# Optimization experiments

Measured on AMD Instinct MI355X. Metric: run time of the kernel, lower is better.

## Reference

```python
import jax, jax.numpy as jnp
import numpy as np

N, C, L, E = 10000, 128, 9, 5  # nodes, channels, (lmax+1)^2, num_elements
INV_SQRT_C = 1.0 / np.sqrt(C).astype(np.float32)


def _sparse(key, shape, p=0.15):
    # mimic the sparsity of e3nn CG coupling (U) tensors
    k1, k2 = jax.random.split(key)
    mask = jax.random.bernoulli(k1, p, shape)
    vals = jax.random.normal(k2, shape, dtype=jnp.float32)
    return jnp.where(mask, vals, 0.0)


def setup_inputs() -> dict:
    key = jax.random.key(0)
    ks = jax.random.split(key, 16)
    node_feats = jax.random.normal(ks[0], (N, C, L), dtype=jnp.float32)
    node_attrs = jax.nn.one_hot(jax.random.randint(ks[1], (N,), 0, E), E, dtype=jnp.float32)
    sc = jax.random.normal(ks[2], (N, 512), dtype=jnp.float32)
    # CG coupling tensors U_nu per output irrep (constant buffers in the torch module)
    # l_out = 0 (d=1): path counts k3=10, k2=3, k1=1
    U3_0 = _sparse(ks[3], (1, L, L, L, 10))
    U2_0 = _sparse(ks[4], (1, L, L, 3))
    U1_0 = _sparse(ks[5], (1, L, 1))
    # l_out = 1 (d=3): path counts k3=12, k2=4, k1=1
    U3_1 = _sparse(ks[6], (3, L, L, L, 12))
    U2_1 = _sparse(ks[7], (3, L, L, 4))
    U1_1 = _sparse(ks[8], (3, L, 1))
    # element-dependent contraction weights: randn(E, k, C) / k  (MACE init)
    w3_0 = jax.random.normal(ks[9], (E, 10, C), dtype=jnp.float32) / 10.0
    w2_0 = jax.random.normal(ks[10], (E, 3, C), dtype=jnp.float32) / 3.0
    w1_0 = jax.random.normal(ks[11], (E, 1, C), dtype=jnp.float32) / 1.0
    w3_1 = jax.random.normal(ks[12], (E, 12, C), dtype=jnp.float32) / 12.0
    w2_1 = jax.random.normal(ks[13], (E, 4, C), dtype=jnp.float32) / 4.0
    w1_1 = jax.random.normal(ks[14], (E, 1, C), dtype=jnp.float32) / 1.0
    # o3.Linear internal weights (one [C,C] block per output irrep)
    kl0, kl1 = jax.random.split(ks[15])
    lin_w0 = jax.random.normal(kl0, (C, C), dtype=jnp.float32)
    lin_w1 = jax.random.normal(kl1, (C, C), dtype=jnp.float32)
    return dict(node_feats=node_feats, node_attrs=node_attrs, sc=sc,
                U3_0=U3_0, U2_0=U2_0, U1_0=U1_0, w3_0=w3_0, w2_0=w2_0, w1_0=w1_0,
                U3_1=U3_1, U2_1=U2_1, U1_1=U1_1, w3_1=w3_1, w2_1=w2_1, w1_1=w1_1,
                lin_w0=lin_w0, lin_w1=lin_w1)


def _contraction(x, y, U3, U2, U1, w3, w2, w1):
    # MACE recursive symmetric contraction, correlation=3.
    # x: [N,C,L] node feats, y: [N,E] one-hot, U_nu: [d, L^nu, k_nu], w_nu: [E,k_nu,C]
    out = jnp.einsum('duvwk,ekc,bcw,be->bcduv', U3, w3, x, y)      # [N,C,d,L,L]
    c2 = jnp.einsum('duvk,ekc,be->bcduv', U2, w2, y) + out
    out = jnp.einsum('bcduv,bcv->bcdu', c2, x)                      # [N,C,d,L]
    c1 = jnp.einsum('duk,ekc,be->bcdu', U1, w1, y) + out
    out = jnp.einsum('bcdu,bcu->bcd', c1, x)                        # [N,C,d]
    return out.reshape(out.shape[0], -1)                            # [N,C*d]


def reference(node_feats, node_attrs, sc,
              U3_0, U2_0, U1_0, w3_0, w2_0, w1_0,
              U3_1, U2_1, U1_1, w3_1, w2_1, w1_1,
              lin_w0, lin_w1):
    # SymmetricContraction: one Contraction per target irrep, concat over irreps
    out0 = _contraction(node_feats, node_attrs, U3_0, U2_0, U1_0, w3_0, w2_0, w1_0)  # [N,C]
    out1 = _contraction(node_feats, node_attrs, U3_1, U2_1, U1_1, w3_1, w2_1, w1_1)  # [N,3C]
    # o3.Linear(target_irreps, target_irreps): per-l channel mixing, 1/sqrt(fan_in)
    y0 = (out0 @ lin_w0) * INV_SQRT_C                                # [N,C]
    x1 = out1.reshape(-1, C, 3)
    y1 = jnp.einsum('bcd,ce->bed', x1, lin_w1) * INV_SQRT_C          # [N,C,3]
    out = jnp.concatenate([y0, y1.reshape(-1, 3 * C)], axis=-1)      # [N,512]
    return out + sc  # use_sc residual
```

## Files before the change

### kernel.cpp

```cpp
#include <hip/hip_runtime.h>


#define CCH 128
#define LDIM 9
#define NE 5
#define BLK 256
#define TSTR 220
#define TGSTR 880
#define U3LDS 8748

__global__ __launch_bounds__(BLK) void count_offs_kernel(
    const float* __restrict__ attrs, int N,
    int* __restrict__ elem, int* __restrict__ gcnt,
    int* __restrict__ offs, int* __restrict__ cur) {
  int n = blockIdx.x * BLK + threadIdx.x;
  int e = 0;
  if (n < N) {
    const float* a = attrs + n * NE;
#pragma unroll
    for (int j = 1; j < NE; ++j)
      if (a[j] > 0.5f) e = j;
    elem[n] = e;
  }
  int lane = threadIdx.x & 63;
#pragma unroll
  for (int k = 0; k < NE; ++k) {
    unsigned long long m = __ballot(n < N && e == k);
    if (m) {
      int leader = __ffsll((long long)m) - 1;
      if (lane == leader) atomicAdd(&gcnt[k], __popcll(m));
    }
  }
  __threadfence();
  __syncthreads();
  if (threadIdx.x == 0) {
    int t = atomicAdd(&gcnt[NE], 1);
    if (t == (int)gridDim.x - 1) {
      int acc = 0;
      for (int k = 0; k < NE; ++k) {
        int ck = atomicAdd(&gcnt[k], 0);
        offs[k] = acc; cur[k] = acc; acc += ck;
      }
      offs[NE] = acc;
    }
  }
}

__global__ __launch_bounds__(BLK) void scatter_kernel(
    const int* __restrict__ elem, int N,
    int* __restrict__ cur, int* __restrict__ order) {
  int n = blockIdx.x * BLK + threadIdx.x;
  if (n >= N) return;
  int e = elem[n];
  int lane = threadIdx.x & 63;
#pragma unroll
  for (int k = 0; k < NE; ++k) {
    if (e == k) {
      unsigned long long m = __ballot(1);
      int cnt = __popcll(m);
      int leader = __ffsll((long long)m) - 1;
      int base = 0;
      if (lane == leader) base = atomicAdd(&cur[k], cnt);
      base = __shfl(base, leader);
      int rank = __popcll(m & ((1ull << lane) - 1ull));
      order[base + rank] = n;
    }
  }
}

__global__ __launch_bounds__(BLK) void table_kernel(
    const float* __restrict__ U3_0, const float* __restrict__ U2_0,
    const float* __restrict__ U1_0, const float* __restrict__ U3_1,
    const float* __restrict__ U2_1, const float* __restrict__ U1_1,
    const float* __restrict__ w3_0, const float* __restrict__ w2_0,
    const float* __restrict__ w1_0, const float* __restrict__ w3_1,
    const float* __restrict__ w2_1, const float* __restrict__ w1_1,
    float* __restrict__ table) {
  const int b = blockIdx.x;
  const int dd = blockIdx.y;
  const int e = b / CCH, c = b % CCH;
  float* Tg = table + (size_t)b * TGSTR + dd * TSTR;
  __shared__ float Us[U3LDS];
  __shared__ float U2s[324];
  __shared__ float R3[729];
  __shared__ float R2[81];
  __shared__ float R1l[9];
  __shared__ float w3l[12], w2l[4];
  const int tid = threadIdx.x;
  const int d = dd - 1;
  const int K3 = (dd == 0) ? 10 : 12;
  const int K2 = (dd == 0) ? 3 : 4;

  if (dd == 0) {
    for (int i = tid; i < 7290; i += BLK) Us[i] = U3_0[i];
    for (int i = tid; i < 243; i += BLK)  U2s[i] = U2_0[i];
    if (tid < 10) w3l[tid] = w3_0[(e * 10 + tid) * CCH + c];
    else if (tid < 13) w2l[tid - 10] = w2_0[(e * 3 + (tid - 10)) * CCH + c];
    if (tid < 9) R1l[tid] = U1_0[tid] * w1_0[e * CCH + c];
  } else {
    for (int i = tid; i < 8748; i += BLK) Us[i] = U3_1[d * 8748 + i];
    for (int i = tid; i < 324; i += BLK)  U2s[i] = U2_1[d * 324 + i];
    if (tid < 12) w3l[tid] = w3_1[(e * 12 + tid) * CCH + c];
    else if (tid < 16) w2l[tid - 12] = w2_1[(e * 4 + (tid - 12)) * CCH + c];
    if (tid < 9) R1l[tid] = U1_1[d * 9 + tid] * w1_1[e * CCH + c];
  }
  __syncthreads();
  for (int r = tid; r < 729; r += BLK) {
    float acc = 0.f;
    for (int k = 0; k < K3; ++k) acc += Us[r * K3 + k] * w3l[k];
    R3[r] = acc;
  }
  for (int q = tid; q < 81; q += BLK) {
    float acc = 0.f;
    for (int k = 0; k < K2; ++k) acc += U2s[q * K2 + k] * w2l[k];
    R2[q] = acc;
  }
  __syncthreads();
  for (int i = tid; i < TSTR; i += BLK) {
    float val = 0.f;
    if (i < 219) {
      int rem = i, u = 0;
      while (rem >= (10 - u) * (11 - u) / 2) {
        rem -= (10 - u) * (11 - u) / 2; ++u;
      }
      if (rem == 0) {
        val = R1l[u];
      } else {
        rem -= 1;
        int v = u;
        while (rem >= 10 - v) { rem -= 10 - v; ++v; }
        if (rem == 0) {
          val = (u == v) ? R2[u * 9 + v] : R2[u * 9 + v] + R2[v * 9 + u];
        } else {
          int w = v + (rem - 1);
          if (u == v && v == w)
            val = R3[(u * 9 + u) * 9 + u];
          else if (u == v)
            val = R3[(u * 9 + u) * 9 + w] + R3[(u * 9 + w) * 9 + u] +
                  R3[(w * 9 + u) * 9 + u];
          else if (v == w)
            val = R3[(u * 9 + v) * 9 + v] + R3[(v * 9 + u) * 9 + v] +
                  R3[(v * 9 + v) * 9 + u];
          else
            val = R3[(u * 9 + v) * 9 + w] + R3[(u * 9 + w) * 9 + v] +
                  R3[(v * 9 + u) * 9 + w] + R3[(v * 9 + w) * 9 + u] +
                  R3[(w * 9 + u) * 9 + v] + R3[(w * 9 + v) * 9 + u];
        }
      }
    }
    Tg[i] = val;
  }
}

__global__ __launch_bounds__(BLK, 8) void contract_kernel(
    const float* __restrict__ feats, const float* __restrict__ table,
    const int* __restrict__ order, const int* __restrict__ offs,
    float* __restrict__ tmp, int NPAD) {
  const int c = blockIdx.x;
  int rem = blockIdx.y;
  int e = -1, pbase = 0, segend = 0;
#pragma unroll
  for (int k = 0; k < NE; ++k) {
    int st = offs[k], en = offs[k + 1];
    int nc = (en - st + BLK - 1) >> 8;
    if (e < 0) {
      if (rem < nc) { e = k; pbase = st + rem * BLK; segend = en; }
      else rem -= nc;
    }
  }
  if (e < 0) return;

  const int p = pbase + threadIdx.x;
  const bool valid = (p < segend);
  const int n = order[valid ? p : (segend - 1)];

  float tf[LDIM];
  {
    const float* xp = feats + ((size_t)n * CCH + c) * LDIM;
#pragma unroll
    for (int q = 0; q < LDIM; ++q) tf[q] = xp[q];
  }

  const float* Tc = table + (size_t)(e * CCH + c) * TGSTR;

#pragma unroll 1
  for (int dd = 0; dd < 4; ++dd) {
    const float* B = Tc + dd * TSTR;
    int idx = 0;
    float acc = 0.f;
#pragma unroll
    for (int u = 0; u < 9; ++u) {
      float inner = B[idx++];
#pragma unroll
      for (int v = u; v < 9; ++v) {
        float Hv = B[idx++];
#pragma unroll
        for (int w = v; w < 9; ++w)
          Hv = fmaf(B[idx++], tf[w], Hv);
        inner = fmaf(Hv, tf[v], inner);
      }
      acc = fmaf(inner, tf[u], acc);
    }
    if (valid) tmp[((size_t)dd * CCH + c) * NPAD + p] = acc;
  }
}

#define NB 16
__global__ __launch_bounds__(BLK, 2) void linear_kernel(
    const float* __restrict__ tmp, const float* __restrict__ W0,
    const float* __restrict__ W1, const float* __restrict__ sc,
    const int* __restrict__ order, float* __restrict__ out, int N, int NPAD) {
  const int p0 = blockIdx.x * NB;
  const int t = threadIdx.x;
  const int wave = t >> 6, lane = t & 63;
  __shared__ __align__(16) float SU[16384];

#pragma unroll
  for (int k = 0; k < 8; ++k) {
    int f = t + k * BLK;
    int dd = f >> 9, r = f & 511;
    int ci = r >> 2, q = r & 3;
    float4 v = *(const float4*)(tmp + (size_t)(dd * CCH + ci) * NPAD + p0 + q * 4);
    *(float4*)(SU + dd * 2048 + ci * 16 + q * 4) = v;
  }
  {
    const int fo0 = wave * 512 + lane * 4;
    const int fo1 = fo0 + 256;
    __builtin_amdgcn_global_load_lds(W0 + fo0, &SU[8192 + fo0], 16, 0, 0);
    __builtin_amdgcn_global_load_lds(W0 + fo1, &SU[8192 + fo1], 16, 0, 0);
    __builtin_amdgcn_global_load_lds(W1 + fo0, &SU[8192 + 2048 + fo0], 16, 0, 0);
    __builtin_amdgcn_global_load_lds(W1 + fo1, &SU[8192 + 2048 + fo1], 16, 0, 0);
  }
  __syncthreads();

  const int j2 = t & 7;
  const int o = t >> 3;
  float acc[2][4][4];
#pragma unroll
  for (int jj = 0; jj < 2; ++jj)
#pragma unroll
    for (int dd = 0; dd < 4; ++dd)
#pragma unroll
      for (int k = 0; k < 4; ++k) acc[jj][dd][k] = 0.f;

#pragma unroll 1
  for (int kk = 0; kk < 8; ++kk) {
    if (kk < 7) {
      const int wb = 8192 + ((kk + 1) & 1) * 4096;
      const float* s0 = W0 + (kk + 1) * 2048;
      const float* s1 = W1 + (kk + 1) * 2048;
      const int fo0 = wave * 512 + lane * 4;
      const int fo1 = fo0 + 256;
      __builtin_amdgcn_global_load_lds(s0 + fo0, &SU[wb + fo0], 16, 0, 0);
      __builtin_amdgcn_global_load_lds(s0 + fo1, &SU[wb + fo1], 16, 0, 0);
      __builtin_amdgcn_global_load_lds(s1 + fo0, &SU[wb + 2048 + fo0], 16, 0, 0);
      __builtin_amdgcn_global_load_lds(s1 + fo1, &SU[wb + 2048 + fo1], 16, 0, 0);
    }
    const int wb = 8192 + (kk & 1) * 4096;
#pragma unroll
    for (int cl = 0; cl < 16; ++cl) {
      const int ci = kk * 16 + cl;
      const float4 wa = *(const float4*)(SU + wb + cl * 128 + o * 4);
      const float4 wc = *(const float4*)(SU + wb + 2048 + cl * 128 + o * 4);
      float av[4][2];
#pragma unroll
      for (int dd = 0; dd < 4; ++dd) {
        av[dd][0] = SU[dd * 2048 + ci * 16 + j2];
        av[dd][1] = SU[dd * 2048 + ci * 16 + j2 + 8];
      }
#pragma unroll
      for (int jj = 0; jj < 2; ++jj) {
        acc[jj][0][0] = fmaf(av[0][jj], wa.x, acc[jj][0][0]);
        acc[jj][0][1] = fmaf(av[0][jj], wa.y, acc[jj][0][1]);
        acc[jj][0][2] = fmaf(av[0][jj], wa.z, acc[jj][0][2]);
        acc[jj][0][3] = fmaf(av[0][jj], wa.w, acc[jj][0][3]);
#pragma unroll
        for (int d = 1; d < 4; ++d) {
          acc[jj][d][0] = fmaf(av[d][jj], wc.x, acc[jj][d][0]);
          acc[jj][d][1] = fmaf(av[d][jj], wc.y, acc[jj][d][1]);
          acc[jj][d][2] = fmaf(av[d][jj], wc.z, acc[jj][d][2]);
          acc[jj][d][3] = fmaf(av[d][jj], wc.w, acc[jj][d][3]);
        }
      }
    }
    __syncthreads();
  }

  const float s = 0.08838834764831843f;
#pragma unroll
  for (int jj = 0; jj < 2; ++jj) {
    float* Sj = SU + (j2 + jj * 8) * 516;
#pragma unroll
    for (int k = 0; k < 4; ++k) {
      int co = o * 4 + k;
      Sj[co]               = acc[jj][0][k] * s;
      Sj[CCH + co * 3 + 0] = acc[jj][1][k] * s;
      Sj[CCH + co * 3 + 1] = acc[jj][2][k] * s;
      Sj[CCH + co * 3 + 2] = acc[jj][3][k] * s;
    }
  }
  __syncthreads();

  const int f = t & 127;
  const int jj4 = t >> 7;
#pragma unroll 1
  for (int jr = jj4; jr < NB; jr += 2) {
    int p = p0 + jr;
    if (p < N) {
      int n = order[p];
      float4 sv = ((const float4*)(sc + (size_t)n * 512))[f];
      float4 ov = ((const float4*)(SU + jr * 516))[f];
      ov.x += sv.x; ov.y += sv.y; ov.z += sv.z; ov.w += sv.w;
      ((float4*)(out + (size_t)n * 512))[f] = ov;
    }
  }
}

extern "C" void kernel_launch(void* const* d_in, const int* in_sizes, int n_in,
                              void* d_out, int out_size, void* d_ws, size_t ws_size,
                              hipStream_t stream) {
  const float* feats = (const float*)d_in[0];
  const float* attrs = (const float*)d_in[1];
  const float* sc    = (const float*)d_in[2];
  const float* U3_0  = (const float*)d_in[3];
  const float* U2_0  = (const float*)d_in[4];
  const float* U1_0  = (const float*)d_in[5];
  const float* w3_0  = (const float*)d_in[6];
  const float* w2_0  = (const float*)d_in[7];
  const float* w1_0  = (const float*)d_in[8];
  const float* U3_1  = (const float*)d_in[9];
  const float* U2_1  = (const float*)d_in[10];
  const float* U1_1  = (const float*)d_in[11];
  const float* w3_1  = (const float*)d_in[12];
  const float* w2_1  = (const float*)d_in[13];
  const float* w1_1  = (const float*)d_in[14];
  const float* W0    = (const float*)d_in[15];
  const float* W1    = (const float*)d_in[16];

  const int N = in_sizes[0] / (CCH * LDIM);
  const int NPAD = ((N + 15) & ~15) + 16;

  float* table = (float*)d_ws;
  float* tmp   = table + (size_t)NE * CCH * TGSTR;
  int*   order = (int*)(tmp + (size_t)4 * CCH * NPAD);
  int*   elem  = order + N;
  int*   offs  = elem + N;
  int*   cur   = offs + 8;
  int*   gcnt  = cur + 8;
  float* out   = (float*)d_out;

  hipMemsetAsync(gcnt, 0, 8 * sizeof(int), stream);

  const int nblk = (N + BLK - 1) / BLK;
  count_offs_kernel<<<dim3(nblk), dim3(BLK), 0, stream>>>(
      attrs, N, elem, gcnt, offs, cur);
  scatter_kernel<<<dim3(nblk), dim3(BLK), 0, stream>>>(elem, N, cur, order);

  table_kernel<<<dim3(NE * CCH, 4), dim3(BLK), 0, stream>>>(
      U3_0, U2_0, U1_0, U3_1, U2_1, U1_1,
      w3_0, w2_0, w1_0, w3_1, w2_1, w1_1, table);

  const int chunksMax = (N + BLK - 1) / BLK + NE;
  contract_kernel<<<dim3(CCH, chunksMax), dim3(BLK), 0, stream>>>(
      feats, table, order, offs, tmp, NPAD);

  linear_kernel<<<dim3((N + NB - 1) / NB), dim3(BLK), 0, stream>>>(
      tmp, W0, W1, sc, order, out, N, NPAD);
}
```

Baseline: 259.5 us.

## Store contraction output node-major and hold linear weights in registers

The contraction kernel now stages its four per-channel results in LDS and writes them as one float4 per node into a node-major [N,512] buffer, replacing the old channel-major padded layout. The linear kernel is rewritten around that layout. Each of 256 blocks of 512 threads owns a contiguous chunk of nodes. Each thread keeps a 128-entry weight column in registers and computes one output per node, reading the intermediate with wave-uniform loads, then adds the skip connection through an LDS row buffer. The aim is to drop the LDS-tiled GEMM staging, but the contraction stores become widely strided across threads. The 128-float register array, under a 512-thread, 2-blocks-per-CU launch bound, risks register spills, and the per-node serial loop gives little parallelism.

```diff
diff --git a/kernel.cpp b/kernel.cpp
--- a/kernel.cpp
+++ b/kernel.cpp
@@ -155,7 +155,7 @@
 __global__ __launch_bounds__(BLK, 8) void contract_kernel(
     const float* __restrict__ feats, const float* __restrict__ table,
     const int* __restrict__ order, const int* __restrict__ offs,
-    float* __restrict__ tmp, int NPAD) {
+    float* __restrict__ tmpT) {
   const int c = blockIdx.x;
   int rem = blockIdx.y;
   int e = -1, pbase = 0, segend = 0;
@@ -174,6 +174,8 @@
   const bool valid = (p < segend);
   const int n = order[valid ? p : (segend - 1)];
 
+  __shared__ float LT[4][BLK];
+
   float tf[LDIM];
   {
     const float* xp = feats + ((size_t)n * CCH + c) * LDIM;
@@ -201,118 +203,84 @@
       }
       acc = fmaf(inner, tf[u], acc);
     }
-    if (valid) tmp[((size_t)dd * CCH + c) * NPAD + p] = acc;
-  }
-}
-
-#define NB 16
-__global__ __launch_bounds__(BLK, 2) void linear_kernel(
-    const float* __restrict__ tmp, const float* __restrict__ W0,
+    LT[dd][threadIdx.x] = acc;
+  }
+  if (valid) {
+    float4 v;
+    v.x = LT[0][threadIdx.x];
+    v.y = LT[1][threadIdx.x];
+    v.z = LT[2][threadIdx.x];
+    v.w = LT[3][threadIdx.x];
+    *(float4*)(tmpT + (size_t)p * 512 + c * 4) = v;
+  }
+}
+
+__global__ __launch_bounds__(512, 2) void linear_kernel(
+    const float* __restrict__ tmpT, const float* __restrict__ W0,
     const float* __restrict__ W1, const float* __restrict__ sc,
-    const int* __restrict__ order, float* __restrict__ out, int N, int NPAD) {
-  const int p0 = blockIdx.x * NB;
+    const int* __restrict__ order, float* __restrict__ out, int N) {
   const int t = threadIdx.x;
-  const int wave = t >> 6, lane = t & 63;
-  __shared__ __align__(16) float SU[16384];
-
-#pragma unroll
-  for (int k = 0; k < 8; ++k) {
-    int f = t + k * BLK;
-    int dd = f >> 9, r = f & 511;
-    int ci = r >> 2, q = r & 3;
-    float4 v = *(const float4*)(tmp + (size_t)(dd * CCH + ci) * NPAD + p0 + q * 4);
-    *(float4*)(SU + dd * 2048 + ci * 16 + q * 4) = v;
-  }
-  {
-    const int fo0 = wave * 512 + lane * 4;
-    const int fo1 = fo0 + 256;
-    __builtin_amdgcn_global_load_lds(W0 + fo0, &SU[8192 + fo0], 16, 0, 0);
-    __builtin_amdgcn_global_load_lds(W0 + fo1, &SU[8192 + fo1], 16, 0, 0);
-    __builtin_amdgcn_global_load_lds(W1 + fo0, &SU[8192 + 2048 + fo0], 16, 0, 0);
-    __builtin_amdgcn_global_load_lds(W1 + fo1, &SU[8192 + 2048 + fo1], 16, 0, 0);
-  }
-  __syncthreads();
-
-  const int j2 = t & 7;
-  const int o = t >> 3;
-  float acc[2][4][4];
-#pragma unroll
-  for (int jj = 0; jj < 2; ++jj)
-#pragma unroll
-    for (int dd = 0; dd < 4; ++dd)
-#pragma unroll
-      for (int k = 0; k < 4; ++k) acc[jj][dd][k] = 0.f;
+  const int pchunk = (N + 255) >> 8;
+  const int pbase = blockIdx.x * pchunk;
+  const int pend  = min(pbase + pchunk, N);
+  if (pbase >= pend) return;
+
+  const int c1 = t & 127;
+  const int dd = __builtin_amdgcn_readfirstlane(t >> 7);
+
+  __shared__ __align__(16) float WS[4096];
+  __shared__ __align__(16) float SROW[8 * 520];
+
+  float wt[128];
+#pragma unroll
+  for (int tile = 0; tile < 8; ++tile) {
+    ((float4*)WS)[t]       = ((const float4*)(W0 + tile * 2048))[t];
+    ((float4*)WS)[512 + t] = ((const float4*)(W1 + tile * 2048))[t];
+    __syncthreads();
+    const float* base = WS + (dd ? 2048 : 0) + c1;
+#pragma unroll
+    for (int k = 0; k < 16; ++k)
+      wt[tile * 16 + k] = base[k * 128];
+    __syncthreads();
+  }
+
+  const int co_map = (dd == 0) ? c1 : (128 + c1 * 3 + (dd - 1));
+  const float s = 0.08838834764831843f;
 
 #pragma unroll 1
-  for (int kk = 0; kk < 8; ++kk) {
-    if (kk < 7) {
-      const int wb = 8192 + ((kk + 1) & 1) * 4096;
-      const float* s0 = W0 + (kk + 1) * 2048;
-      const float* s1 = W1 + (kk + 1) * 2048;
-      const int fo0 = wave * 512 + lane * 4;
-      const int fo1 = fo0 + 256;
-      __builtin_amdgcn_global_load_lds(s0 + fo0, &SU[wb + fo0], 16, 0, 0);
-      __builtin_amdgcn_global_load_lds(s0 + fo1, &SU[wb + fo1], 16, 0, 0);
-      __builtin_amdgcn_global_load_lds(s1 + fo0, &SU[wb + 2048 + fo0], 16, 0, 0);
-      __builtin_amdgcn_global_load_lds(s1 + fo1, &SU[wb + 2048 + fo1], 16, 0, 0);
-    }
-    const int wb = 8192 + (kk & 1) * 4096;
-#pragma unroll
-    for (int cl = 0; cl < 16; ++cl) {
-      const int ci = kk * 16 + cl;
-      const float4 wa = *(const float4*)(SU + wb + cl * 128 + o * 4);
-      const float4 wc = *(const float4*)(SU + wb + 2048 + cl * 128 + o * 4);
-      float av[4][2];
-#pragma unroll
-      for (int dd = 0; dd < 4; ++dd) {
-        av[dd][0] = SU[dd * 2048 + ci * 16 + j2];
-        av[dd][1] = SU[dd * 2048 + ci * 16 + j2 + 8];
-      }
-#pragma unroll
-      for (int jj = 0; jj < 2; ++jj) {
-        acc[jj][0][0] = fmaf(av[0][jj], wa.x, acc[jj][0][0]);
-        acc[jj][0][1] = fmaf(av[0][jj], wa.y, acc[jj][0][1]);
-        acc[jj][0][2] = fmaf(av[0][jj], wa.z, acc[jj][0][2]);
-        acc[jj][0][3] = fmaf(av[0][jj], wa.w, acc[jj][0][3]);
-#pragma unroll
-        for (int d = 1; d < 4; ++d) {
-          acc[jj][d][0] = fmaf(av[d][jj], wc.x, acc[jj][d][0]);
-          acc[jj][d][1] = fmaf(av[d][jj], wc.y, acc[jj][d][1]);
-          acc[jj][d][2] = fmaf(av[d][jj], wc.z, acc[jj][d][2]);
-          acc[jj][d][3] = fmaf(av[d][jj], wc.w, acc[jj][d][3]);
+  for (int pb = pbase; pb < pend; pb += 8) {
+#pragma unroll 1
+    for (int i = 0; i < 8; ++i) {
+      const int p = pb + i;
+      if (p < pend) {
+        const float* Ad = tmpT + (size_t)p * 512 + dd;
+        float acc = 0.f;
+#pragma unroll
+        for (int cc = 0; cc < 32; ++cc) {
+#pragma unroll
+          for (int j = 0; j < 4; ++j)
+            acc = fmaf(wt[cc * 4 + j], Ad[cc * 16 + j * 4], acc);
         }
+        SROW[i * 520 + co_map] = acc * s;
       }
     }
     __syncthreads();
-  }
-
-  const float s = 0.08838834764831843f;
-#pragma unroll
-  for (int jj = 0; jj < 2; ++jj) {
-    float* Sj = SU + (j2 + jj * 8) * 516;
-#pragma unroll
-    for (int k = 0; k < 4; ++k) {
-      int co = o * 4 + k;
-      Sj[co]               = acc[jj][0][k] * s;
-      Sj[CCH + co * 3 + 0] = acc[jj][1][k] * s;
-      Sj[CCH + co * 3 + 1] = acc[jj][2][k] * s;
-      Sj[CCH + co * 3 + 2] = acc[jj][3][k] * s;
-    }
-  }
-  __syncthreads();
-
-  const int f = t & 127;
-  const int jj4 = t >> 7;
-#pragma unroll 1
-  for (int jr = jj4; jr < NB; jr += 2) {
-    int p = p0 + jr;
-    if (p < N) {
-      int n = order[p];
-      float4 sv = ((const float4*)(sc + (size_t)n * 512))[f];
-      float4 ov = ((const float4*)(SU + jr * 516))[f];
-      ov.x += sv.x; ov.y += sv.y; ov.z += sv.z; ov.w += sv.w;
-      ((float4*)(out + (size_t)n * 512))[f] = ov;
-    }
+    const int r = t >> 6, f = t & 63;
+    const int p2 = pb + r;
+    if (p2 < pend) {
+      const int n = order[p2];
+      const float4* scp = (const float4*)(sc + (size_t)n * 512);
+      float4* op = (float4*)(out + (size_t)n * 512);
+#pragma unroll
+      for (int q = 0; q < 2; ++q) {
+        const int idx = f + q * 64;
+        float4 v = *(const float4*)(SROW + r * 520 + idx * 4);
+        float4 s4 = scp[idx];
+        v.x += s4.x; v.y += s4.y; v.z += s4.z; v.w += s4.w;
+        op[idx] = v;
+      }
+    }
+    __syncthreads();
   }
 }
 
@@ -338,11 +306,10 @@
   const float* W1    = (const float*)d_in[16];
 
   const int N = in_sizes[0] / (CCH * LDIM);
-  const int NPAD = ((N + 15) & ~15) + 16;
 
   float* table = (float*)d_ws;
-  float* tmp   = table + (size_t)NE * CCH * TGSTR;
-  int*   order = (int*)(tmp + (size_t)4 * CCH * NPAD);
+  float* tmpT  = table + (size_t)NE * CCH * TGSTR;
+  int*   order = (int*)(tmpT + (size_t)N * 512);
   int*   elem  = order + N;
   int*   offs  = elem + N;
   int*   cur   = offs + 8;
@@ -362,8 +329,8 @@
 
   const int chunksMax = (N + BLK - 1) / BLK + NE;
   contract_kernel<<<dim3(CCH, chunksMax), dim3(BLK), 0, stream>>>(
-      feats, table, order, offs, tmp, NPAD);
-
-  linear_kernel<<<dim3((N + NB - 1) / NB), dim3(BLK), 0, stream>>>(
-      tmp, W0, W1, sc, order, out, N, NPAD);
-}
+      feats, table, order, offs, tmpT);
+
+  linear_kernel<<<dim3(256), dim3(512), 0, stream>>>(
+      tmpT, W0, W1, sc, order, out, N);
+}
```

Result: slower. 433.5 us (+67.1%).

## Retile linear kernel to 32 nodes per block with 8x8 register tiles

Applied to the files above, without the earlier changes.

Restructures the channel-mixing GEMM so each block handles 32 nodes instead of 16, and each thread keeps an 8x8 accumulator tile (one wave per output component d) instead of a 2x4x4 tile. Both the activation tile and the weight tile are now streamed into LDS with double-buffered direct global-to-LDS loads, so activation loads overlap compute the way weight loads already did. The aim is more FMAs per LDS load and half as many weight reloads per node. In exchange it needs 64 accumulator registers per thread, an epilogue split into two halves, and reads of tmp past N that rely on NPAD padding covering 32-node blocks.

```diff
diff --git a/kernel.cpp b/kernel.cpp
--- a/kernel.cpp
+++ b/kernel.cpp
@@ -205,115 +205,117 @@
   }
 }
 
-#define NB 16
+#define LNB 32
 __global__ __launch_bounds__(BLK, 2) void linear_kernel(
     const float* __restrict__ tmp, const float* __restrict__ W0,
     const float* __restrict__ W1, const float* __restrict__ sc,
     const int* __restrict__ order, float* __restrict__ out, int N, int NPAD) {
-  const int p0 = blockIdx.x * NB;
+  const int p0 = blockIdx.x * LNB;
   const int t = threadIdx.x;
   const int wave = t >> 6, lane = t & 63;
-  __shared__ __align__(16) float SU[16384];
-
-#pragma unroll
-  for (int k = 0; k < 8; ++k) {
-    int f = t + k * BLK;
-    int dd = f >> 9, r = f & 511;
-    int ci = r >> 2, q = r & 3;
-    float4 v = *(const float4*)(tmp + (size_t)(dd * CCH + ci) * NPAD + p0 + q * 4);
-    *(float4*)(SU + dd * 2048 + ci * 16 + q * 4) = v;
-  }
-  {
-    const int fo0 = wave * 512 + lane * 4;
-    const int fo1 = fo0 + 256;
-    __builtin_amdgcn_global_load_lds(W0 + fo0, &SU[8192 + fo0], 16, 0, 0);
-    __builtin_amdgcn_global_load_lds(W0 + fo1, &SU[8192 + fo1], 16, 0, 0);
-    __builtin_amdgcn_global_load_lds(W1 + fo0, &SU[8192 + 2048 + fo0], 16, 0, 0);
-    __builtin_amdgcn_global_load_lds(W1 + fo1, &SU[8192 + 2048 + fo1], 16, 0, 0);
-  }
+  __shared__ __align__(16) float LB[12288];
+
+  const int nq = t & 3;
+  const int oq = (t >> 2) & 15;
+  const int dd = wave;
+
+#define ISSUE_A(KK, B)                                                       \
+  {                                                                          \
+    float* Ab = LB + (B) * 2048;                                             \
+    _Pragma("unroll")                                                        \
+    for (int qq = 0; qq < 2; ++qq) {                                         \
+      const int q = wave * 2 + qq;                                           \
+      const int row = q * 8 + (lane >> 3);                                   \
+      const int ci = (KK) * 16 + (row >> 2);                                 \
+      const float* src = tmp +                                               \
+          ((size_t)((row & 3) * CCH + ci) * NPAD + p0) + (lane & 7) * 4;     \
+      __builtin_amdgcn_global_load_lds(src, Ab + q * 256 + lane * 4, 16, 0, 0); \
+    }                                                                        \
+  }
+#define ISSUE_W(KK, B)                                                       \
+  {                                                                          \
+    float* Wb = LB + 4096 + (B) * 4096;                                      \
+    _Pragma("unroll")                                                        \
+    for (int qq = 0; qq < 4; ++qq) {                                         \
+      const int q = wave * 4 + qq;                                           \
+      const int row = q * 2 + (lane >> 5);                                   \
+      const int ci = (KK) * 16 + (row >> 1);                                 \
+      const float* src =                                                     \
+          ((row & 1) ? W1 : W0) + (size_t)ci * CCH + (lane & 31) * 4;        \
+      __builtin_amdgcn_global_load_lds(src, Wb + q * 256 + lane * 4, 16, 0, 0); \
+    }                                                                        \
+  }
+
+  ISSUE_A(0, 0)
+  ISSUE_W(0, 0)
   __syncthreads();
 
-  const int j2 = t & 7;
-  const int o = t >> 3;
-  float acc[2][4][4];
-#pragma unroll
-  for (int jj = 0; jj < 2; ++jj)
-#pragma unroll
-    for (int dd = 0; dd < 4; ++dd)
-#pragma unroll
-      for (int k = 0; k < 4; ++k) acc[jj][dd][k] = 0.f;
+  float acc[8][8];
+#pragma unroll
+  for (int r = 0; r < 8; ++r)
+#pragma unroll
+    for (int k = 0; k < 8; ++k) acc[r][k] = 0.f;
 
 #pragma unroll 1
   for (int kk = 0; kk < 8; ++kk) {
     if (kk < 7) {
-      const int wb = 8192 + ((kk + 1) & 1) * 4096;
-      const float* s0 = W0 + (kk + 1) * 2048;
-      const float* s1 = W1 + (kk + 1) * 2048;
-      const int fo0 = wave * 512 + lane * 4;
-      const int fo1 = fo0 + 256;
-      __builtin_amdgcn_global_load_lds(s0 + fo0, &SU[wb + fo0], 16, 0, 0);
-      __builtin_amdgcn_global_load_lds(s0 + fo1, &SU[wb + fo1], 16, 0, 0);
-      __builtin_amdgcn_global_load_lds(s1 + fo0, &SU[wb + 2048 + fo0], 16, 0, 0);
-      __builtin_amdgcn_global_load_lds(s1 + fo1, &SU[wb + 2048 + fo1], 16, 0, 0);
-    }
-    const int wb = 8192 + (kk & 1) * 4096;
-#pragma unroll
+      ISSUE_A(kk + 1, (kk + 1) & 1)
+      ISSUE_W(kk + 1, (kk + 1) & 1)
+    }
+    const float* Ab = LB + (kk & 1) * 2048;
+    const float* Wb = LB + 4096 + (kk & 1) * 4096;
+#pragma unroll 2
     for (int cl = 0; cl < 16; ++cl) {
-      const int ci = kk * 16 + cl;
-      const float4 wa = *(const float4*)(SU + wb + cl * 128 + o * 4);
-      const float4 wc = *(const float4*)(SU + wb + 2048 + cl * 128 + o * 4);
-      float av[4][2];
-#pragma unroll
-      for (int dd = 0; dd < 4; ++dd) {
-        av[dd][0] = SU[dd * 2048 + ci * 16 + j2];
-        av[dd][1] = SU[dd * 2048 + ci * 16 + j2 + 8];
-      }
-#pragma unroll
-      for (int jj = 0; jj < 2; ++jj) {
-        acc[jj][0][0] = fmaf(av[0][jj], wa.x, acc[jj][0][0]);
-        acc[jj][0][1] = fmaf(av[0][jj], wa.y, acc[jj][0][1]);
-        acc[jj][0][2] = fmaf(av[0][jj], wa.z, acc[jj][0][2]);
-        acc[jj][0][3] = fmaf(av[0][jj], wa.w, acc[jj][0][3]);
-#pragma unroll
-        for (int d = 1; d < 4; ++d) {
-          acc[jj][d][0] = fmaf(av[d][jj], wc.x, acc[jj][d][0]);
-          acc[jj][d][1] = fmaf(av[d][jj], wc.y, acc[jj][d][1]);
-          acc[jj][d][2] = fmaf(av[d][jj], wc.z, acc[jj][d][2]);
-          acc[jj][d][3] = fmaf(av[d][jj], wc.w, acc[jj][d][3]);
+      const float* ap = Ab + (cl * 4 + dd) * 32 + nq * 8;
+      const float* wp = Wb + (cl * 2 + (dd ? 1 : 0)) * 128 + oq * 8;
+      const float4 a0 = *(const float4*)(ap);
+      const float4 a1 = *(const float4*)(ap + 4);
+      const float4 w0 = *(const float4*)(wp);
+      const float4 w1 = *(const float4*)(wp + 4);
+      const float a[8] = {a0.x, a0.y, a0.z, a0.w, a1.x, a1.y, a1.z, a1.w};
+      const float w[8] = {w0.x, w0.y, w0.z, w0.w, w1.x, w1.y, w1.z, w1.w};
+#pragma unroll
+      for (int r = 0; r < 8; ++r)
+#pragma unroll
+        for (int k = 0; k < 8; ++k)
+          acc[r][k] = fmaf(a[r], w[k], acc[r][k]);
+    }
+    __syncthreads();
+  }
+
+  const float s = 0.08838834764831843f;
+#pragma unroll 1
+  for (int hb = 0; hb < 2; ++hb) {
+    if ((nq >> 1) == hb) {
+      const int rbase = (nq & 1) * 8;
+#pragma unroll
+      for (int r = 0; r < 8; ++r) {
+        float* Sj = LB + (rbase + r) * 520;
+#pragma unroll
+        for (int k = 0; k < 8; ++k) {
+          const int co = oq * 8 + k;
+          if (dd == 0) Sj[co] = acc[r][k] * s;
+          else         Sj[CCH + co * 3 + (dd - 1)] = acc[r][k] * s;
         }
       }
     }
     __syncthreads();
-  }
-
-  const float s = 0.08838834764831843f;
-#pragma unroll
-  for (int jj = 0; jj < 2; ++jj) {
-    float* Sj = SU + (j2 + jj * 8) * 516;
-#pragma unroll
-    for (int k = 0; k < 4; ++k) {
-      int co = o * 4 + k;
-      Sj[co]               = acc[jj][0][k] * s;
-      Sj[CCH + co * 3 + 0] = acc[jj][1][k] * s;
-      Sj[CCH + co * 3 + 1] = acc[jj][2][k] * s;
-      Sj[CCH + co * 3 + 2] = acc[jj][3][k] * s;
-    }
-  }
-  __syncthreads();
-
-  const int f = t & 127;
-  const int jj4 = t >> 7;
+    const int f = t & 127, rr = t >> 7;
 #pragma unroll 1
-  for (int jr = jj4; jr < NB; jr += 2) {
-    int p = p0 + jr;
-    if (p < N) {
-      int n = order[p];
-      float4 sv = ((const float4*)(sc + (size_t)n * 512))[f];
-      float4 ov = ((const float4*)(SU + jr * 516))[f];
-      ov.x += sv.x; ov.y += sv.y; ov.z += sv.z; ov.w += sv.w;
-      ((float4*)(out + (size_t)n * 512))[f] = ov;
-    }
-  }
+    for (int jr = rr; jr < 16; jr += 2) {
+      const int p = p0 + hb * 16 + jr;
+      if (p < N) {
+        const int n = order[p];
+        float4 sv = ((const float4*)(sc + (size_t)n * 512))[f];
+        float4 ov = *(const float4*)(LB + jr * 520 + f * 4);
+        ov.x += sv.x; ov.y += sv.y; ov.z += sv.z; ov.w += sv.w;
+        ((float4*)(out + (size_t)n * 512))[f] = ov;
+      }
+    }
+    __syncthreads();
+  }
+#undef ISSUE_A
+#undef ISSUE_W
 }
 
 extern "C" void kernel_launch(void* const* d_in, const int* in_sizes, int n_in,
@@ -364,6 +366,6 @@
   contract_kernel<<<dim3(CCH, chunksMax), dim3(BLK), 0, stream>>>(
       feats, table, order, offs, tmp, NPAD);
 
-  linear_kernel<<<dim3((N + NB - 1) / NB), dim3(BLK), 0, stream>>>(
+  linear_kernel<<<dim3((N + LNB - 1) / LNB), dim3(BLK), 0, stream>>>(
       tmp, W0, W1, sc, order, out, N, NPAD);
 }
```

Result: faster. 252.7 us (-2.6%).
